# Kernel optimization log

Hardware: AMD Instinct MI355X
Metric: run time of the kernel (lower is better)

The kernel has to match this reference:

```python
import jax, jax.numpy as jnp
import numpy as np

N_EMBED = 384
NUM_HEADS = 6
HEAD_SIZE = 64
B, T = 128, 256


def setup_inputs() -> dict:
    key = jax.random.key(0)
    ks = jax.random.split(key, 6)
    x = jax.random.normal(ks[0], (B, T, N_EMBED), dtype=jnp.float32)
    s = 0.02
    Wq = jax.random.normal(ks[1], (NUM_HEADS, N_EMBED, HEAD_SIZE), dtype=jnp.float32) * s
    Wk = jax.random.normal(ks[2], (NUM_HEADS, N_EMBED, HEAD_SIZE), dtype=jnp.float32) * s
    Wv = jax.random.normal(ks[3], (NUM_HEADS, N_EMBED, HEAD_SIZE), dtype=jnp.float32) * s
    Wp = jax.random.normal(ks[4], (NUM_HEADS * HEAD_SIZE, N_EMBED), dtype=jnp.float32) * s
    bp = jnp.zeros((N_EMBED,), dtype=jnp.float32)
    return {"x": x, "Wq": Wq, "Wk": Wk, "Wv": Wv, "Wp": Wp, "bp": bp}


def reference(x, Wq, Wk, Wv, Wp, bp):
    # x: [B,T,C]; Wq/Wk/Wv: [H,C,hs]; Wp: [H*hs, C]
    Bx, Tx, C = x.shape
    q = jnp.einsum('btc,hcd->bhtd', x, Wq)
    k = jnp.einsum('btc,hcd->bhtd', x, Wk)
    v = jnp.einsum('btc,hcd->bhtd', x, Wv)
    scale = HEAD_SIZE ** (-0.5)
    scores = jnp.einsum('bhtd,bhsd->bhts', q, k) * scale  # [B,H,T,T]
    causal = jnp.tril(jnp.ones((Tx, Tx), dtype=bool))
    scores = jnp.where(causal, scores, -jnp.inf)
    attn = jax.nn.softmax(scores, axis=-1)
    # dropout is identity in eval mode
    out = jnp.einsum('bhts,bhsd->bhtd', attn, v)  # [B,H,T,hs]
    out = out.transpose(0, 2, 1, 3).reshape(Bx, Tx, NUM_HEADS * HEAD_SIZE)
    return out @ Wp + bp
```

## Files before the change

kernel.cpp:

```cpp
#include <hip/hip_runtime.h>
#include <hip/hip_bf16.h>

#define C_DIM 384
#define H_NUM 6
#define HS    64
#define B_DIM 128
#define T_DIM 256
#define NROWS (B_DIM * T_DIM)

typedef unsigned short u16;
typedef unsigned int u32;
typedef short bf16x8 __attribute__((ext_vector_type(8)));
typedef float floatx4 __attribute__((ext_vector_type(4)));

__device__ __forceinline__ u16 f2b(float f) {
  __hip_bfloat16 h = __float2bfloat16(f);
  u16 u;
  __builtin_memcpy(&u, &h, 2);
  return u;
}
__device__ __forceinline__ void gload_lds16(const void* g, void* lds) {
  __builtin_amdgcn_global_load_lds(
      (const __attribute__((address_space(1))) u32*)g,
      (__attribute__((address_space(3))) u32*)lds, 16, 0, 0);
}

__global__ __launch_bounds__(256) void prep_kernel(
    const float* __restrict__ x, const float* __restrict__ Wq,
    const float* __restrict__ Wk, const float* __restrict__ Wv,
    const float* __restrict__ Wp, u16* __restrict__ xb,
    u16* __restrict__ Wh, u16* __restrict__ Wpt) {
  const int bid = blockIdx.x;
  const int tid = threadIdx.x;
  if (bid < 6144) {
    const int i = bid * 256 + tid;
    const float4 f0 = ((const float4*)x)[i * 2];
    const float4 f1 = ((const float4*)x)[i * 2 + 1];
    bf16x8 pk;
    pk[0] = (short)f2b(f0.x); pk[1] = (short)f2b(f0.y);
    pk[2] = (short)f2b(f0.z); pk[3] = (short)f2b(f0.w);
    pk[4] = (short)f2b(f1.x); pk[5] = (short)f2b(f1.y);
    pk[6] = (short)f2b(f1.z); pk[7] = (short)f2b(f1.w);
    ((bf16x8*)xb)[i] = pk;
  } else {
    const int idx = (bid - 6144) * 256 + tid;
    const int WHN = H_NUM * 192 * C_DIM;
    if (idx < WHN) {
      int h = idx / (192 * C_DIM);
      int rem = idx % (192 * C_DIM);
      int r = rem / C_DIM, c = rem % C_DIM;
      int tz = r >> 6, d = r & 63;
      const float* W = (tz == 0) ? Wq : (tz == 1) ? Wk : Wv;
      Wh[idx] = f2b(W[((size_t)h * C_DIM + c) * HS + d]);
    } else {
      int j = idx - WHN;
      int n = j / C_DIM, c = j % C_DIM;
      Wpt[j] = f2b(Wp[c * C_DIM + n]);
    }
  }
}

#define QS_OFF  0
#define KLS_OFF 16384
#define VTS_OFF 32768
#define PLS_OFF 49152

template <bool DIAG>
__device__ __forceinline__ void attn_chunk_f(int c, int mt, int lane, int ln,
                                             int qd, const bf16x8* qf,
                                             const u16* smem, u16* Pw,
                                             floatx4* oacc, float* lsum) {
  floatx4 sacc[4];
#pragma unroll
  for (int st = 0; st < 4; ++st) {
    sacc[st] = floatx4{0.f, 0.f, 0.f, 0.f};
#pragma unroll
    for (int kc = 0; kc < 2; ++kc) {
      bf16x8 kf = *(const bf16x8*)&smem[KLS_OFF + ((c * 4 + st) * 2 + kc) * 512 +
                                        lane * 8];
      sacc[st] =
          __builtin_amdgcn_mfma_f32_16x16x32_bf16(qf[kc], kf, sacc[st], 0, 0, 0);
    }
  }
#pragma unroll
  for (int st = 0; st < 4; ++st) {
#pragma unroll
    for (int r = 0; r < 4; ++r) {
      const float sv = sacc[st][r] * 0.125f;
      float p = __expf(sv);
      if (DIAG) {
        const bool ok = (c * 64 + st * 16 + ln) <= (mt * 16 + qd * 4 + r);
        p = ok ? p : 0.f;
      }
      lsum[r] += p;
      Pw[(qd * 4 + r) * 72 + st * 16 + ln] = f2b(p);
    }
  }
#pragma unroll
  for (int kc2 = 0; kc2 < 2; ++kc2) {
    bf16x8 pf = *(const bf16x8*)&Pw[ln * 72 + kc2 * 32 + qd * 8];
#pragma unroll
    for (int dt = 0; dt < 4; ++dt) {
      bf16x8 vf = *(const bf16x8*)&smem[VTS_OFF + (dt * 16 + ln) * 256 +
                                        ((c * 64 + kc2 * 32 + qd * 8) ^
                                         ((ln & 7) << 3))];
      oacc[dt] =
          __builtin_amdgcn_mfma_f32_16x16x32_bf16(pf, vf, oacc[dt], 0, 0, 0);
    }
  }
}

__global__ __launch_bounds__(512) void qkv_attn_fused(
    const u16* __restrict__ xb, const u16* __restrict__ Wh,
    u16* __restrict__ y) {
  __shared__ __align__(16) u16 smem[58368];
  const int b = blockIdx.x;
  const int h = blockIdx.y;
  const u16* a_rows = xb + (size_t)b * 256 * C_DIM;
  const u16* wbase = Wh + (size_t)h * 192 * C_DIM;

  const int tid = threadIdx.x;
  const int lane = tid & 63;
  const int w = tid >> 6;
  const int lr = lane >> 3;
  const int lkc = (lane & 7) * 8;
  const int qd = lane >> 4;
  const int ln = lane & 15;
  const int wm = (w >> 1) * 64;
  const int wn = (w & 1) * 96;

  floatx4 acc[4][6];
#pragma unroll
  for (int i = 0; i < 4; ++i)
#pragma unroll
    for (int j = 0; j < 6; ++j) acc[i][j] = floatx4{0.f, 0.f, 0.f, 0.f};

  for (int kb = 0; kb < C_DIM / 64; ++kb) {
    const int k0 = kb * 64;
    __syncthreads();
#pragma unroll
    for (int s = 0; s < 4; ++s) {
      const int rbase = (s * 8 + w) * 8;
      gload_lds16(a_rows + (size_t)(rbase + lr) * C_DIM + k0 + lkc,
                  smem + rbase * 64);
    }
#pragma unroll
    for (int s = 0; s < 3; ++s) {
      const int rbase = (s * 8 + w) * 8;
      gload_lds16(wbase + (size_t)(rbase + lr) * C_DIM + k0 + lkc,
                  smem + KLS_OFF + rbase * 64);
    }
    __syncthreads();

#pragma unroll
    for (int kk = 0; kk < 2; ++kk) {
      bf16x8 af[4], bf[6];
#pragma unroll
      for (int mt = 0; mt < 4; ++mt)
        af[mt] =
            *(const bf16x8*)&smem[(wm + mt * 16 + ln) * 64 + kk * 32 + qd * 8];
#pragma unroll
      for (int nt = 0; nt < 6; ++nt)
        bf[nt] = *(const bf16x8*)&smem[KLS_OFF + (wn + nt * 16 + ln) * 64 +
                                       kk * 32 + qd * 8];
#pragma unroll
      for (int mt = 0; mt < 4; ++mt)
#pragma unroll
        for (int nt = 0; nt < 6; ++nt)
          acc[mt][nt] = __builtin_amdgcn_mfma_f32_16x16x32_bf16(
              af[mt], bf[nt], acc[mt][nt], 0, 0, 0);
    }
  }
  __syncthreads();

#pragma unroll
  for (int nt = 0; nt < 6; ++nt) {
    const int c0 = wn + nt * 16;
#pragma unroll
    for (int mt = 0; mt < 4; ++mt) {
#pragma unroll
      for (int r = 0; r < 4; ++r) {
        const int t = wm + mt * 16 + qd * 4 + r;
        const u16 val = f2b(acc[mt][nt][r]);
        if (c0 < 64) {
          smem[QS_OFF + t * 64 + c0 + ln] = val;
        } else if (c0 < 128) {
          const int d = c0 - 64 + ln;
          smem[KLS_OFF + ((t >> 4) << 10) + ((d >> 5) << 9) +
               (((d >> 3) & 3) << 7) + ((t & 15) << 3) + (d & 7)] = val;
        } else {
          const int dv = c0 - 128 + ln;
          smem[VTS_OFF + dv * 256 + (t ^ ((dv & 7) << 3))] = val;
        }
      }
    }
  }
  __syncthreads();

  u16* Pw = smem + PLS_OFF + w * 1152;
#pragma unroll
  for (int i = 0; i < 2; ++i) {
    const int mt = i ? (15 - w) : w;
    bf16x8 qf[2];
#pragma unroll
    for (int kc = 0; kc < 2; ++kc)
      qf[kc] = *(const bf16x8*)&smem[QS_OFF + (mt * 16 + ln) * 64 + kc * 32 +
                                     qd * 8];

    floatx4 oacc[4];
    float lsum[4];
#pragma unroll
    for (int dt = 0; dt < 4; ++dt) oacc[dt] = floatx4{0.f, 0.f, 0.f, 0.f};
#pragma unroll
    for (int r = 0; r < 4; ++r) lsum[r] = 0.f;

    const int cmax = mt >> 2;
    for (int c = 0; c < cmax; ++c)
      attn_chunk_f<false>(c, mt, lane, ln, qd, qf, smem, Pw, oacc, lsum);
    attn_chunk_f<true>(cmax, mt, lane, ln, qd, qf, smem, Pw, oacc, lsum);

#pragma unroll
    for (int off = 1; off < 16; off <<= 1)
#pragma unroll
      for (int r = 0; r < 4; ++r) lsum[r] += __shfl_xor(lsum[r], off);

#pragma unroll
    for (int r = 0; r < 4; ++r) {
      const float inv = 1.f / lsum[r];
      const int t = mt * 16 + qd * 4 + r;
      u16* yo = y + ((size_t)b * T_DIM + t) * C_DIM + h * HS;
#pragma unroll
      for (int dt = 0; dt < 4; ++dt) yo[dt * 16 + ln] = f2b(oacc[dt][r] * inv);
    }
  }
}

__global__ __launch_bounds__(256) void proj_gemm(
    const u16* __restrict__ yb, const u16* __restrict__ Wpt,
    const float* __restrict__ bp, float* __restrict__ out) {
  __shared__ u16 As[128 * 64];
  __shared__ u16 Bs[128 * 64];
  const int row0 = blockIdx.x * 128;
  const int n0 = blockIdx.y * 128;
  const u16* a_rows = yb + (size_t)row0 * C_DIM;
  const u16* bt_rows = Wpt + (size_t)n0 * C_DIM;

  const int tid = threadIdx.x;
  const int lane = tid & 63;
  const int w = tid >> 6;
  const int lr = lane >> 3;
  const int lkc = (lane & 7) * 8;
  const int qd = lane >> 4;
  const int ln = lane & 15;
  const int mw = (w >> 1) * 64;
  const int nw = (w & 1) * 64;

  floatx4 acc[4][4];
#pragma unroll
  for (int i = 0; i < 4; ++i)
#pragma unroll
    for (int j = 0; j < 4; ++j) acc[i][j] = floatx4{0.f, 0.f, 0.f, 0.f};

  for (int kb = 0; kb < C_DIM / 64; ++kb) {
    const int k0 = kb * 64;
    __syncthreads();
#pragma unroll
    for (int s = 0; s < 4; ++s) {
      const int rbase = (s * 4 + w) * 8;
      gload_lds16(a_rows + (size_t)(rbase + lr) * C_DIM + k0 + lkc,
                  As + rbase * 64);
      gload_lds16(bt_rows + (size_t)(rbase + lr) * C_DIM + k0 + lkc,
                  Bs + rbase * 64);
    }
    __syncthreads();

#pragma unroll
    for (int kk = 0; kk < 2; ++kk) {
      bf16x8 af[4], bf[4];
#pragma unroll
      for (int mt = 0; mt < 4; ++mt)
        af[mt] = *(const bf16x8*)&As[(mw + mt * 16 + ln) * 64 + kk * 32 + qd * 8];
#pragma unroll
      for (int nt = 0; nt < 4; ++nt)
        bf[nt] = *(const bf16x8*)&Bs[(nw + nt * 16 + ln) * 64 + kk * 32 + qd * 8];
#pragma unroll
      for (int mt = 0; mt < 4; ++mt)
#pragma unroll
        for (int nt = 0; nt < 4; ++nt)
          acc[mt][nt] = __builtin_amdgcn_mfma_f32_16x16x32_bf16(
              af[mt], bf[nt], acc[mt][nt], 0, 0, 0);
    }
  }

#pragma unroll
  for (int nt = 0; nt < 4; ++nt) {
    const int col = n0 + nw + nt * 16 + ln;
    const float bias = bp[col];
#pragma unroll
    for (int mt = 0; mt < 4; ++mt) {
#pragma unroll
      for (int r = 0; r < 4; ++r) {
        const int grow = row0 + mw + mt * 16 + qd * 4 + r;
        out[(size_t)grow * C_DIM + col] = acc[mt][nt][r] + bias;
      }
    }
  }
}

extern "C" void kernel_launch(void* const* d_in, const int* in_sizes, int n_in,
                              void* d_out, int out_size, void* d_ws, size_t ws_size,
                              hipStream_t stream) {
  const float* x  = (const float*)d_in[0];
  const float* Wq = (const float*)d_in[1];
  const float* Wk = (const float*)d_in[2];
  const float* Wv = (const float*)d_in[3];
  const float* Wp = (const float*)d_in[4];
  const float* bp = (const float*)d_in[5];
  float* out = (float*)d_out;

  const size_t n_x = (size_t)NROWS * C_DIM;

  u16* Wh  = (u16*)d_ws;
  u16* Wpt = Wh + (size_t)H_NUM * 192 * C_DIM;
  u16* xb  = Wpt + C_DIM * C_DIM;
  u16* y   = xb + n_x;

  prep_kernel<<<6144 + 2304, 256, 0, stream>>>(x, Wq, Wk, Wv, Wp, xb, Wh, Wpt);
  qkv_attn_fused<<<dim3(B_DIM, H_NUM), 512, 0, stream>>>(xb, Wh, y);
  proj_gemm<<<dim3(NROWS / 128, 3), 256, 0, stream>>>(y, Wpt, bp, out);
}
```

Measured before the change: 199.8 us.

## Fuse x bf16 conversion into QKV kernel and XOR-swizzle LDS tiles

```diff
diff --git a/kernel.cpp b/kernel.cpp
--- a/kernel.cpp
+++ b/kernel.cpp
@@ -25,38 +25,25 @@
       (__attribute__((address_space(3))) u32*)lds, 16, 0, 0);
 }
 
-__global__ __launch_bounds__(256) void prep_kernel(
-    const float* __restrict__ x, const float* __restrict__ Wq,
-    const float* __restrict__ Wk, const float* __restrict__ Wv,
-    const float* __restrict__ Wp, u16* __restrict__ xb,
+__global__ __launch_bounds__(256) void prep_w(
+    const float* __restrict__ Wq, const float* __restrict__ Wk,
+    const float* __restrict__ Wv, const float* __restrict__ Wp,
     u16* __restrict__ Wh, u16* __restrict__ Wpt) {
-  const int bid = blockIdx.x;
-  const int tid = threadIdx.x;
-  if (bid < 6144) {
-    const int i = bid * 256 + tid;
-    const float4 f0 = ((const float4*)x)[i * 2];
-    const float4 f1 = ((const float4*)x)[i * 2 + 1];
-    bf16x8 pk;
-    pk[0] = (short)f2b(f0.x); pk[1] = (short)f2b(f0.y);
-    pk[2] = (short)f2b(f0.z); pk[3] = (short)f2b(f0.w);
-    pk[4] = (short)f2b(f1.x); pk[5] = (short)f2b(f1.y);
-    pk[6] = (short)f2b(f1.z); pk[7] = (short)f2b(f1.w);
-    ((bf16x8*)xb)[i] = pk;
+  const int idx = blockIdx.x * 256 + threadIdx.x;
+  const int WHN = H_NUM * 192 * C_DIM;
+  if (idx < WHN) {
+    int h = idx / (192 * C_DIM);
+    int rem = idx % (192 * C_DIM);
+    int r = rem / C_DIM, c = rem % C_DIM;
+    int tz = r >> 6, d = r & 63;
+    const int cs = c ^ ((r & 7) << 3);
+    const float* W = (tz == 0) ? Wq : (tz == 1) ? Wk : Wv;
+    Wh[idx] = f2b(W[((size_t)h * C_DIM + cs) * HS + d]);
   } else {
-    const int idx = (bid - 6144) * 256 + tid;
-    const int WHN = H_NUM * 192 * C_DIM;
-    if (idx < WHN) {
-      int h = idx / (192 * C_DIM);
-      int rem = idx % (192 * C_DIM);
-      int r = rem / C_DIM, c = rem % C_DIM;
-      int tz = r >> 6, d = r & 63;
-      const float* W = (tz == 0) ? Wq : (tz == 1) ? Wk : Wv;
-      Wh[idx] = f2b(W[((size_t)h * C_DIM + c) * HS + d]);
-    } else {
-      int j = idx - WHN;
-      int n = j / C_DIM, c = j % C_DIM;
-      Wpt[j] = f2b(Wp[c * C_DIM + n]);
-    }
+    int j = idx - WHN;
+    int n = j / C_DIM, c = j % C_DIM;
+    const int cs = c ^ ((n & 7) << 3);
+    Wpt[j] = f2b(Wp[cs * C_DIM + n]);
   }
 }
 
@@ -110,13 +97,24 @@
   }
 }
 
+#define A_ISSUE(K0)                                                     \
+  {                                                                     \
+    _Pragma("unroll") for (int u = 0; u < 4; ++u) {                     \
+      const int idx_ = u * 512 + tid;                                   \
+      const int row_ = idx_ >> 3, c8_ = (idx_ & 7) * 8;                 \
+      const float* p_ = xg + (size_t)row_ * C_DIM + (K0) + c8_;         \
+      ar[2 * u] = *(const float4*)p_;                                   \
+      ar[2 * u + 1] = *(const float4*)(p_ + 4);                         \
+    }                                                                   \
+  }
+
 __global__ __launch_bounds__(512) void qkv_attn_fused(
-    const u16* __restrict__ xb, const u16* __restrict__ Wh,
+    const float* __restrict__ x, const u16* __restrict__ Wh,
     u16* __restrict__ y) {
   __shared__ __align__(16) u16 smem[58368];
   const int b = blockIdx.x;
   const int h = blockIdx.y;
-  const u16* a_rows = xb + (size_t)b * 256 * C_DIM;
+  const float* xg = x + (size_t)b * 256 * C_DIM;
   const u16* wbase = Wh + (size_t)h * 192 * C_DIM;
 
   const int tid = threadIdx.x;
@@ -126,6 +124,7 @@
   const int lkc = (lane & 7) * 8;
   const int qd = lane >> 4;
   const int ln = lane & 15;
+  const int sx = (ln & 7) << 3;
   const int wm = (w >> 1) * 64;
   const int wn = (w & 1) * 96;
 
@@ -135,15 +134,27 @@
 #pragma unroll
     for (int j = 0; j < 6; ++j) acc[i][j] = floatx4{0.f, 0.f, 0.f, 0.f};
 
-  for (int kb = 0; kb < C_DIM / 64; ++kb) {
+  float4 ar[8];
+  A_ISSUE(0);
+
+  for (int kb = 0; kb < 6; ++kb) {
+    __syncthreads();
+#pragma unroll
+    for (int u = 0; u < 4; ++u) {
+      const int idx_ = u * 512 + tid;
+      const int row_ = idx_ >> 3, c8_ = (idx_ & 7) * 8;
+      bf16x8 pk;
+      pk[0] = (short)f2b(ar[2 * u].x);
+      pk[1] = (short)f2b(ar[2 * u].y);
+      pk[2] = (short)f2b(ar[2 * u].z);
+      pk[3] = (short)f2b(ar[2 * u].w);
+      pk[4] = (short)f2b(ar[2 * u + 1].x);
+      pk[5] = (short)f2b(ar[2 * u + 1].y);
+      pk[6] = (short)f2b(ar[2 * u + 1].z);
+      pk[7] = (short)f2b(ar[2 * u + 1].w);
+      *(bf16x8*)&smem[QS_OFF + row_ * 64 + (c8_ ^ ((row_ & 7) << 3))] = pk;
+    }
     const int k0 = kb * 64;
-    __syncthreads();
-#pragma unroll
-    for (int s = 0; s < 4; ++s) {
-      const int rbase = (s * 8 + w) * 8;
-      gload_lds16(a_rows + (size_t)(rbase + lr) * C_DIM + k0 + lkc,
-                  smem + rbase * 64);
-    }
 #pragma unroll
     for (int s = 0; s < 3; ++s) {
       const int rbase = (s * 8 + w) * 8;
@@ -151,18 +162,19 @@
                   smem + KLS_OFF + rbase * 64);
     }
     __syncthreads();
+    if (kb < 5) A_ISSUE((kb + 1) * 64);
 
 #pragma unroll
     for (int kk = 0; kk < 2; ++kk) {
       bf16x8 af[4], bf[6];
 #pragma unroll
       for (int mt = 0; mt < 4; ++mt)
-        af[mt] =
-            *(const bf16x8*)&smem[(wm + mt * 16 + ln) * 64 + kk * 32 + qd * 8];
+        af[mt] = *(const bf16x8*)&smem[QS_OFF + (wm + mt * 16 + ln) * 64 +
+                                       ((kk * 32 + qd * 8) ^ sx)];
 #pragma unroll
       for (int nt = 0; nt < 6; ++nt)
         bf[nt] = *(const bf16x8*)&smem[KLS_OFF + (wn + nt * 16 + ln) * 64 +
-                                       kk * 32 + qd * 8];
+                                       ((kk * 32 + qd * 8) ^ sx)];
 #pragma unroll
       for (int mt = 0; mt < 4; ++mt)
 #pragma unroll
@@ -228,9 +240,11 @@
     for (int r = 0; r < 4; ++r) {
       const float inv = 1.f / lsum[r];
       const int t = mt * 16 + qd * 4 + r;
+      const int sy = (t & 7) << 3;
       u16* yo = y + ((size_t)b * T_DIM + t) * C_DIM + h * HS;
 #pragma unroll
-      for (int dt = 0; dt < 4; ++dt) yo[dt * 16 + ln] = f2b(oacc[dt][r] * inv);
+      for (int dt = 0; dt < 4; ++dt)
+        yo[(dt * 16 + ln) ^ sy] = f2b(oacc[dt][r] * inv);
     }
   }
 }
@@ -252,6 +266,7 @@
   const int lkc = (lane & 7) * 8;
   const int qd = lane >> 4;
   const int ln = lane & 15;
+  const int sx = (ln & 7) << 3;
   const int mw = (w >> 1) * 64;
   const int nw = (w & 1) * 64;
 
@@ -279,10 +294,12 @@
       bf16x8 af[4], bf[4];
 #pragma unroll
       for (int mt = 0; mt < 4; ++mt)
-        af[mt] = *(const bf16x8*)&As[(mw + mt * 16 + ln) * 64 + kk * 32 + qd * 8];
+        af[mt] = *(const bf16x8*)&As[(mw + mt * 16 + ln) * 64 +
+                                     ((kk * 32 + qd * 8) ^ sx)];
 #pragma unroll
       for (int nt = 0; nt < 4; ++nt)
-        bf[nt] = *(const bf16x8*)&Bs[(nw + nt * 16 + ln) * 64 + kk * 32 + qd * 8];
+        bf[nt] = *(const bf16x8*)&Bs[(nw + nt * 16 + ln) * 64 +
+                                     ((kk * 32 + qd * 8) ^ sx)];
 #pragma unroll
       for (int mt = 0; mt < 4; ++mt)
 #pragma unroll
@@ -318,14 +335,11 @@
   const float* bp = (const float*)d_in[5];
   float* out = (float*)d_out;
 
-  const size_t n_x = (size_t)NROWS * C_DIM;
-
   u16* Wh  = (u16*)d_ws;
   u16* Wpt = Wh + (size_t)H_NUM * 192 * C_DIM;
-  u16* xb  = Wpt + C_DIM * C_DIM;
-  u16* y   = xb + n_x;
-
-  prep_kernel<<<6144 + 2304, 256, 0, stream>>>(x, Wq, Wk, Wv, Wp, xb, Wh, Wpt);
-  qkv_attn_fused<<<dim3(B_DIM, H_NUM), 512, 0, stream>>>(xb, Wh, y);
+  u16* y   = Wpt + C_DIM * C_DIM;
+
+  prep_w<<<2304, 256, 0, stream>>>(Wq, Wk, Wv, Wp, Wh, Wpt);
+  qkv_attn_fused<<<dim3(B_DIM, H_NUM), 512, 0, stream>>>(x, Wh, y);
   proj_gemm<<<dim3(NROWS / 128, 3), 256, 0, stream>>>(y, Wpt, bp, out);
 }
```

Result: faster. 191.9 us (-4.0%).

## Double-buffer QKV GEMM loads and XOR-swizzle bf16 layouts to avoid LDS bank conflicts

Applied to the files above, without the earlier changes.

```diff
diff --git a/kernel.cpp b/kernel.cpp
--- a/kernel.cpp
+++ b/kernel.cpp
@@ -34,8 +34,12 @@
   const int tid = threadIdx.x;
   if (bid < 6144) {
     const int i = bid * 256 + tid;
-    const float4 f0 = ((const float4*)x)[i * 2];
-    const float4 f1 = ((const float4*)x)[i * 2 + 1];
+    const int row = (i * 8) / C_DIM;
+    const int c8 = (i * 8) % C_DIM;
+    const int cs = c8 ^ ((row & 7) << 3);
+    const float* p = x + (size_t)row * C_DIM + cs;
+    const float4 f0 = *(const float4*)p;
+    const float4 f1 = *(const float4*)(p + 4);
     bf16x8 pk;
     pk[0] = (short)f2b(f0.x); pk[1] = (short)f2b(f0.y);
     pk[2] = (short)f2b(f0.z); pk[3] = (short)f2b(f0.w);
@@ -50,16 +54,22 @@
       int rem = idx % (192 * C_DIM);
       int r = rem / C_DIM, c = rem % C_DIM;
       int tz = r >> 6, d = r & 63;
+      const int cs = c ^ ((r & 7) << 3);
       const float* W = (tz == 0) ? Wq : (tz == 1) ? Wk : Wv;
-      Wh[idx] = f2b(W[((size_t)h * C_DIM + c) * HS + d]);
+      Wh[idx] = f2b(W[((size_t)h * C_DIM + cs) * HS + d]);
     } else {
       int j = idx - WHN;
       int n = j / C_DIM, c = j % C_DIM;
-      Wpt[j] = f2b(Wp[c * C_DIM + n]);
-    }
-  }
-}
-
+      const int cs = c ^ ((n & 7) << 3);
+      Wpt[j] = f2b(Wp[cs * C_DIM + n]);
+    }
+  }
+}
+
+#define AS0_OFF 0
+#define AS1_OFF 16384
+#define BS0_OFF 32768
+#define BS1_OFF 45056
 #define QS_OFF  0
 #define KLS_OFF 16384
 #define VTS_OFF 32768
@@ -126,6 +136,7 @@
   const int lkc = (lane & 7) * 8;
   const int qd = lane >> 4;
   const int ln = lane & 15;
+  const int sx = (ln & 7) << 3;
   const int wm = (w >> 1) * 64;
   const int wn = (w & 1) * 96;
 
@@ -135,34 +146,56 @@
 #pragma unroll
     for (int j = 0; j < 6; ++j) acc[i][j] = floatx4{0.f, 0.f, 0.f, 0.f};
 
-  for (int kb = 0; kb < C_DIM / 64; ++kb) {
-    const int k0 = kb * 64;
-    __syncthreads();
-#pragma unroll
-    for (int s = 0; s < 4; ++s) {
-      const int rbase = (s * 8 + w) * 8;
-      gload_lds16(a_rows + (size_t)(rbase + lr) * C_DIM + k0 + lkc,
-                  smem + rbase * 64);
-    }
-#pragma unroll
-    for (int s = 0; s < 3; ++s) {
-      const int rbase = (s * 8 + w) * 8;
-      gload_lds16(wbase + (size_t)(rbase + lr) * C_DIM + k0 + lkc,
-                  smem + KLS_OFF + rbase * 64);
-    }
-    __syncthreads();
+#pragma unroll
+  for (int s = 0; s < 4; ++s) {
+    const int rbase = (s * 8 + w) * 8;
+    gload_lds16(a_rows + (size_t)(rbase + lr) * C_DIM + lkc,
+                smem + AS0_OFF + rbase * 64);
+  }
+#pragma unroll
+  for (int s = 0; s < 3; ++s) {
+    const int rbase = (s * 8 + w) * 8;
+    gload_lds16(wbase + (size_t)(rbase + lr) * C_DIM + lkc,
+                smem + BS0_OFF + rbase * 64);
+  }
+
+  for (int kb = 0; kb < 6; ++kb) {
+    const int pa = (kb & 1) ? AS1_OFF : AS0_OFF;
+    const int pb = (kb & 1) ? BS1_OFF : BS0_OFF;
+    if (kb < 5) {
+      const int qa = (kb & 1) ? AS0_OFF : AS1_OFF;
+      const int qb = (kb & 1) ? BS0_OFF : BS1_OFF;
+      const int k0 = (kb + 1) * 64;
+#pragma unroll
+      for (int s = 0; s < 4; ++s) {
+        const int rbase = (s * 8 + w) * 8;
+        gload_lds16(a_rows + (size_t)(rbase + lr) * C_DIM + k0 + lkc,
+                    smem + qa + rbase * 64);
+      }
+#pragma unroll
+      for (int s = 0; s < 3; ++s) {
+        const int rbase = (s * 8 + w) * 8;
+        gload_lds16(wbase + (size_t)(rbase + lr) * C_DIM + k0 + lkc,
+                    smem + qb + rbase * 64);
+      }
+      asm volatile("s_waitcnt vmcnt(7)" ::: "memory");
+    } else {
+      asm volatile("s_waitcnt vmcnt(0)" ::: "memory");
+    }
+    __builtin_amdgcn_s_barrier();
+    __builtin_amdgcn_sched_barrier(0);
 
 #pragma unroll
     for (int kk = 0; kk < 2; ++kk) {
       bf16x8 af[4], bf[6];
 #pragma unroll
       for (int mt = 0; mt < 4; ++mt)
-        af[mt] =
-            *(const bf16x8*)&smem[(wm + mt * 16 + ln) * 64 + kk * 32 + qd * 8];
+        af[mt] = *(const bf16x8*)&smem[pa + (wm + mt * 16 + ln) * 64 +
+                                       ((kk * 32 + qd * 8) ^ sx)];
 #pragma unroll
       for (int nt = 0; nt < 6; ++nt)
-        bf[nt] = *(const bf16x8*)&smem[KLS_OFF + (wn + nt * 16 + ln) * 64 +
-                                       kk * 32 + qd * 8];
+        bf[nt] = *(const bf16x8*)&smem[pb + (wn + nt * 16 + ln) * 64 +
+                                       ((kk * 32 + qd * 8) ^ sx)];
 #pragma unroll
       for (int mt = 0; mt < 4; ++mt)
 #pragma unroll
@@ -170,8 +203,9 @@
           acc[mt][nt] = __builtin_amdgcn_mfma_f32_16x16x32_bf16(
               af[mt], bf[nt], acc[mt][nt], 0, 0, 0);
     }
-  }
-  __syncthreads();
+    __builtin_amdgcn_sched_barrier(0);
+    __builtin_amdgcn_s_barrier();
+  }
 
 #pragma unroll
   for (int nt = 0; nt < 6; ++nt) {
@@ -228,9 +262,11 @@
     for (int r = 0; r < 4; ++r) {
       const float inv = 1.f / lsum[r];
       const int t = mt * 16 + qd * 4 + r;
+      const int sy = (t & 7) << 3;
       u16* yo = y + ((size_t)b * T_DIM + t) * C_DIM + h * HS;
 #pragma unroll
-      for (int dt = 0; dt < 4; ++dt) yo[dt * 16 + ln] = f2b(oacc[dt][r] * inv);
+      for (int dt = 0; dt < 4; ++dt)
+        yo[(dt * 16 + ln) ^ sy] = f2b(oacc[dt][r] * inv);
     }
   }
 }
@@ -252,6 +288,7 @@
   const int lkc = (lane & 7) * 8;
   const int qd = lane >> 4;
   const int ln = lane & 15;
+  const int sx = (ln & 7) << 3;
   const int mw = (w >> 1) * 64;
   const int nw = (w & 1) * 64;
 
@@ -279,10 +316,12 @@
       bf16x8 af[4], bf[4];
 #pragma unroll
       for (int mt = 0; mt < 4; ++mt)
-        af[mt] = *(const bf16x8*)&As[(mw + mt * 16 + ln) * 64 + kk * 32 + qd * 8];
+        af[mt] = *(const bf16x8*)&As[(mw + mt * 16 + ln) * 64 +
+                                     ((kk * 32 + qd * 8) ^ sx)];
 #pragma unroll
       for (int nt = 0; nt < 4; ++nt)
-        bf[nt] = *(const bf16x8*)&Bs[(nw + nt * 16 + ln) * 64 + kk * 32 + qd * 8];
+        bf[nt] = *(const bf16x8*)&Bs[(nw + nt * 16 + ln) * 64 +
+                                     ((kk * 32 + qd * 8) ^ sx)];
 #pragma unroll
       for (int mt = 0; mt < 4; ++mt)
 #pragma unroll
```

Result: faster. 181.9 us (-9.0%).
